# Kernel tuning notes

Measured on AMD Instinct MI355X. Metric: run time of the kernel, lower is better.

Reference implementation:

```python
import jax, jax.numpy as jnp
import numpy as np

B = 4096          # batch_size
D = 256           # embedding dim
N = 2 * B
TEMPERATURE = 0.5
GAMMA = 2.0
ALPHA = 0.25


def _negative_indices():
    # Static column indices of negatives per row: all columns except self (i)
    # and the positive partner ((i+B) mod N). Shape (N, N-2).
    idx = []
    for i in range(N):
        partner = (i + B) % N
        cols = [j for j in range(N) if j != i and j != partner]
        idx.append(cols)
    return np.asarray(idx, dtype=np.int32)

_NEG_IDX = jnp.asarray(_negative_indices())


def setup_inputs() -> dict:
    key = jax.random.key(0)
    kx, ky = jax.random.split(key)
    zx = jax.random.normal(kx, (B, D), dtype=jnp.float32)
    zy = jax.random.normal(ky, (B, D), dtype=jnp.float32)
    return {"zx": zx, "zy": zy}


def reference(zx, zy):
    z = jnp.concatenate([zx, zy], axis=0)                    # (N, D)
    zn = z / jnp.linalg.norm(z, axis=1, keepdims=True)       # cosine normalize
    sim = (zn @ zn.T) / TEMPERATURE                          # (N, N)

    sim_xy = jnp.diagonal(sim, offset=B)                     # (B,)
    sim_yx = jnp.diagonal(sim, offset=-B)                    # (B,)
    pos = jnp.concatenate([sim_xy, sim_yx])[:, None]         # (N, 1)
    neg = jnp.take_along_axis(sim, _NEG_IDX, axis=1)         # (N, N-2)

    logits = jnp.concatenate([pos, neg], axis=1)             # (N, N-1)
    # CE with label 0 for every row: -log_softmax(logits)[:, 0]
    ce = jax.nn.logsumexp(logits, axis=1) - logits[:, 0]
    pt = jnp.exp(-ce)
    focal = (1.0 - pt) ** GAMMA * ce
    return (ALPHA * focal).mean()
```

## Files before the change

### kernel.cpp

```cpp
#include <hip/hip_runtime.h>
#include <stdint.h>
#include <stddef.h>


typedef __attribute__((ext_vector_type(8))) short short8;
typedef __attribute__((ext_vector_type(4))) float f32x4;

#define NROWS 8192
#define DDIM 256
#define NTILES 2080

__device__ __forceinline__ unsigned short f2bf(float f) {
  unsigned int u = __float_as_uint(f);
  u = (u + 0x7FFFu + ((u >> 16) & 1u)) >> 16;
  return (unsigned short)u;
}

__global__ __launch_bounds__(256) void norm_kernel(const float* __restrict__ zx,
                                                   const float* __restrict__ zy,
                                                   unsigned short* __restrict__ zn) {
  const int row = blockIdx.x * 4 + (threadIdx.x >> 6);
  const int lane = threadIdx.x & 63;
  const float* src = (row < 4096) ? (zx + (size_t)row * DDIM)
                                  : (zy + (size_t)(row - 4096) * DDIM);
  float4 v = reinterpret_cast<const float4*>(src)[lane];
  float ss = v.x * v.x + v.y * v.y + v.z * v.z + v.w * v.w;
#pragma unroll
  for (int m = 1; m < 64; m <<= 1) ss += __shfl_xor(ss, m);
  const float sc = 1.41421356237f * rsqrtf(ss);
  ushort4 o;
  o.x = f2bf(v.x * sc); o.y = f2bf(v.y * sc);
  o.z = f2bf(v.z * sc); o.w = f2bf(v.w * sc);
  reinterpret_cast<ushort4*>(zn + (size_t)row * DDIM)[lane] = o;
}

__global__ __launch_bounds__(256, 2) void simtri_kernel(const unsigned short* __restrict__ zn,
                                                        float* __restrict__ partial,
                                                        float* __restrict__ pos) {
  __shared__ unsigned short smem[2][2][128 * 64];
  const int bid = blockIdx.x;
  int p = (int)((129.0f - sqrtf((float)(16641 - 8 * bid))) * 0.5f);
  p = max(0, min(63, p));
  while ((((p + 1) * (129 - (p + 1))) >> 1) <= bid) ++p;
  while (((p * (129 - p)) >> 1) > bid) --p;
  const int q = p + (bid - ((p * (129 - p)) >> 1));
  const int R0 = p << 7;
  const int C0 = q << 7;
  const bool isdiag = (p == q);
  const bool ispos = (q == p + 32);

  const int tid = threadIdx.x;
  const int lane = tid & 63;
  const int wid = tid >> 6;
  const int wr = wid >> 1;
  const int wc = wid & 1;

  const f32x4 z4 = {0.f, 0.f, 0.f, 0.f};
  f32x4 acc[4][4];
#pragma unroll
  for (int m = 0; m < 4; ++m)
#pragma unroll
    for (int n = 0; n < 4; ++n) acc[m][n] = z4;

  auto stage = [&](int buf, int which, int row0, int k0) {
    unsigned short* lb = &smem[buf][which][0];
#pragma unroll
    for (int j = 0; j < 4; ++j) {
      const int u = j * 256 + wid * 64 + lane;
      const unsigned short* g = zn + (size_t)(row0 + (u >> 3)) * DDIM + k0 + (u & 7) * 8;
      unsigned short* l = lb + (size_t)(j * 256 + wid * 64) * 8;
      __builtin_amdgcn_global_load_lds(
          (const __attribute__((address_space(1))) void*)g,
          (__attribute__((address_space(3))) void*)l, 16, 0, 0);
    }
  };

  stage(0, 0, R0, 0);
  if (!isdiag) stage(0, 1, C0, 0);
  __syncthreads();

  int buf = 0;
#pragma unroll
  for (int s = 0; s < 4; ++s) {
    if (s < 3) {
      stage(buf ^ 1, 0, R0, (s + 1) * 64);
      if (!isdiag) stage(buf ^ 1, 1, C0, (s + 1) * 64);
    }
    const unsigned short* A = &smem[buf][0][0];
    const unsigned short* Bm = isdiag ? A : &smem[buf][1][0];
#pragma unroll
    for (int ks = 0; ks < 2; ++ks) {
      short8 af[4], bfr[4];
#pragma unroll
      for (int m = 0; m < 4; ++m)
        af[m] = *reinterpret_cast<const short8*>(
            A + ((wr * 64 + m * 16 + (lane & 15)) * 64 + ks * 32 + (lane >> 4) * 8));
#pragma unroll
      for (int n = 0; n < 4; ++n)
        bfr[n] = *reinterpret_cast<const short8*>(
            Bm + ((wc * 64 + n * 16 + (lane & 15)) * 64 + ks * 32 + (lane >> 4) * 8));
#pragma unroll
      for (int m = 0; m < 4; ++m)
#pragma unroll
        for (int n = 0; n < 4; ++n)
          acc[m][n] = __builtin_amdgcn_mfma_f32_16x16x32_bf16(af[m], bfr[n], acc[m][n], 0, 0, 0);
    }
    buf ^= 1;
    __syncthreads();
  }

  float rsum[4][4];
  float csum[4];
#pragma unroll
  for (int m = 0; m < 4; ++m)
#pragma unroll
    for (int r = 0; r < 4; ++r) rsum[m][r] = 0.f;
#pragma unroll
  for (int n = 0; n < 4; ++n) csum[n] = 0.f;

#pragma unroll
  for (int m = 0; m < 4; ++m) {
    const int grow_b = R0 + wr * 64 + m * 16 + ((lane >> 4) << 2);
#pragma unroll
    for (int n = 0; n < 4; ++n) {
      const int gcol = C0 + wc * 64 + n * 16 + (lane & 15);
#pragma unroll
      for (int r = 0; r < 4; ++r) {
        const int grow = grow_b + r;
        const float val = acc[m][n][r];
        if (ispos && (gcol == grow + 4096)) pos[grow] = val;
        const float e = (isdiag && (grow == gcol)) ? 0.f : __expf(val);
        rsum[m][r] += e;
        csum[n] += e;
      }
    }
  }

#pragma unroll
  for (int m = 0; m < 4; ++m)
#pragma unroll
    for (int r = 0; r < 4; ++r) {
      float s = rsum[m][r];
      s += __shfl_xor(s, 1); s += __shfl_xor(s, 2);
      s += __shfl_xor(s, 4); s += __shfl_xor(s, 8);
      if ((lane & 15) == 0) {
        const int grow = R0 + wr * 64 + m * 16 + ((lane >> 4) << 2) + r;
        partial[(size_t)(q * 2 + wc) * NROWS + grow] = s;
      }
    }

  if (!isdiag) {
#pragma unroll
    for (int n = 0; n < 4; ++n) {
      float c = csum[n];
      c += __shfl_xor(c, 16); c += __shfl_xor(c, 32);
      if (lane < 16)
        partial[(size_t)(p * 2 + wr) * NROWS + (C0 + wc * 64 + n * 16 + lane)] = c;
    }
  }
}

__global__ __launch_bounds__(256) void d1_kernel(const float* __restrict__ partial,
                                                 const float* __restrict__ pos,
                                                 float* __restrict__ bsum) {
  const int row = blockIdx.x * 256 + threadIdx.x;
  float s = 0.f;
#pragma unroll 16
  for (int c = 0; c < 128; ++c) s += partial[(size_t)c * NROWS + row];
  const float ce = __logf(s) - pos[row & 4095];
  const float pt = __expf(-ce);
  float f = (1.f - pt) * (1.f - pt) * ce;
#pragma unroll
  for (int m = 1; m < 64; m <<= 1) f += __shfl_xor(f, m);
  __shared__ float wsum[4];
  if ((threadIdx.x & 63) == 0) wsum[threadIdx.x >> 6] = f;
  __syncthreads();
  if (threadIdx.x == 0) bsum[blockIdx.x] = wsum[0] + wsum[1] + wsum[2] + wsum[3];
}

__global__ __launch_bounds__(64) void d2_kernel(const float* __restrict__ bsum,
                                                float* __restrict__ out) {
  const int l = threadIdx.x;
  float v = (l < 32) ? bsum[l] : 0.f;
#pragma unroll
  for (int m = 1; m < 64; m <<= 1) v += __shfl_xor(v, m);
  if (l == 0) out[0] = 0.25f * v / 8192.f;
}

extern "C" void kernel_launch(void* const* d_in, const int* in_sizes, int n_in,
                              void* d_out, int out_size, void* d_ws, size_t ws_size,
                              hipStream_t stream) {
  const float* zx = (const float*)d_in[0];
  const float* zy = (const float*)d_in[1];
  float* out = (float*)d_out;

  unsigned short* zn = (unsigned short*)d_ws;
  float* pos = (float*)((char*)d_ws + (size_t)NROWS * DDIM * 2);
  float* partial = pos + 4096;
  float* bsum = partial + (size_t)128 * NROWS;

  norm_kernel<<<2048, 256, 0, stream>>>(zx, zy, zn);
  simtri_kernel<<<NTILES, 256, 0, stream>>>(zn, partial, pos);
  d1_kernel<<<32, 256, 0, stream>>>(partial, pos, bsum);
  d2_kernel<<<1, 64, 0, stream>>>(bsum, out);
}
```

Measured before the change: 112.6 us.

## Persistent tile loop with cross-tile prefetch, exp2 scaling, fused final reduction

The similarity kernel becomes persistent: 512 blocks each walk 4-5 triangular tiles and prefetch the next tile's first K-slice while the current tile finishes. Before this, 2080 short-lived blocks each paid their own prologue and epilogue. The normalization scale now folds in log2(e), so the kernel can use a raw exp2, and the diagonal and positive-pair handling moves out of the per-element loop into a targeted correction. The last reduction kernel is merged into d1 through an atomic counter that norm_kernel resets. This removes one launch but relies on the counter reset ordering and on a fixed tile distribution across 256 CUs.

```diff
diff --git a/kernel.cpp b/kernel.cpp
--- a/kernel.cpp
+++ b/kernel.cpp
@@ -9,6 +9,7 @@
 #define NROWS 8192
 #define DDIM 256
 #define NTILES 2080
+#define NBLK 512
 
 __device__ __forceinline__ unsigned short f2bf(float f) {
   unsigned int u = __float_as_uint(f);
@@ -16,9 +17,20 @@
   return (unsigned short)u;
 }
 
+__device__ __forceinline__ void unrank_tile(int t, int& p_out, int& q_out) {
+  int p = (int)((129.0f - sqrtf((float)(16641 - 8 * t))) * 0.5f);
+  p = max(0, min(63, p));
+  while ((((p + 1) * (129 - (p + 1))) >> 1) <= t) ++p;
+  while (((p * (129 - p)) >> 1) > t) --p;
+  p_out = p;
+  q_out = p + (t - ((p * (129 - p)) >> 1));
+}
+
 __global__ __launch_bounds__(256) void norm_kernel(const float* __restrict__ zx,
                                                    const float* __restrict__ zy,
-                                                   unsigned short* __restrict__ zn) {
+                                                   unsigned short* __restrict__ zn,
+                                                   unsigned int* __restrict__ counter) {
+  if (blockIdx.x == 0 && threadIdx.x == 0) *counter = 0u;
   const int row = blockIdx.x * 4 + (threadIdx.x >> 6);
   const int lane = threadIdx.x & 63;
   const float* src = (row < 4096) ? (zx + (size_t)row * DDIM)
@@ -27,7 +39,7 @@
   float ss = v.x * v.x + v.y * v.y + v.z * v.z + v.w * v.w;
 #pragma unroll
   for (int m = 1; m < 64; m <<= 1) ss += __shfl_xor(ss, m);
-  const float sc = 1.41421356237f * rsqrtf(ss);
+  const float sc = 1.69864360f * rsqrtf(ss);
   ushort4 o;
   o.x = f2bf(v.x * sc); o.y = f2bf(v.y * sc);
   o.z = f2bf(v.z * sc); o.w = f2bf(v.w * sc);
@@ -39,16 +51,7 @@
                                                         float* __restrict__ pos) {
   __shared__ unsigned short smem[2][2][128 * 64];
   const int bid = blockIdx.x;
-  int p = (int)((129.0f - sqrtf((float)(16641 - 8 * bid))) * 0.5f);
-  p = max(0, min(63, p));
-  while ((((p + 1) * (129 - (p + 1))) >> 1) <= bid) ++p;
-  while (((p * (129 - p)) >> 1) > bid) --p;
-  const int q = p + (bid - ((p * (129 - p)) >> 1));
-  const int R0 = p << 7;
-  const int C0 = q << 7;
-  const bool isdiag = (p == q);
-  const bool ispos = (q == p + 32);
-
+  const int nt = (bid < NTILES - NBLK * 4) ? 5 : 4;
   const int tid = threadIdx.x;
   const int lane = tid & 63;
   const int wid = tid >> 6;
@@ -62,7 +65,7 @@
 #pragma unroll
     for (int n = 0; n < 4; ++n) acc[m][n] = z4;
 
-  auto stage = [&](int buf, int which, int row0, int k0) {
+  auto stage_one = [&](int buf, int which, int row0, int k0) {
     unsigned short* lb = &smem[buf][which][0];
 #pragma unroll
     for (int j = 0; j < 4; ++j) {
@@ -74,117 +77,147 @@
           (__attribute__((address_space(3))) void*)l, 16, 0, 0);
     }
   };
-
-  stage(0, 0, R0, 0);
-  if (!isdiag) stage(0, 1, C0, 0);
+  auto stageT = [&](int buf, int p, int q, int k0) {
+    stage_one(buf, 0, p << 7, k0);
+    if (p != q) stage_one(buf, 1, q << 7, k0);
+  };
+
+  int cp, cq;
+  unrank_tile(bid, cp, cq);
+  stageT(0, cp, cq, 0);
   __syncthreads();
 
   int buf = 0;
-#pragma unroll
-  for (int s = 0; s < 4; ++s) {
-    if (s < 3) {
-      stage(buf ^ 1, 0, R0, (s + 1) * 64);
-      if (!isdiag) stage(buf ^ 1, 1, C0, (s + 1) * 64);
-    }
-    const unsigned short* A = &smem[buf][0][0];
-    const unsigned short* Bm = isdiag ? A : &smem[buf][1][0];
-#pragma unroll
-    for (int ks = 0; ks < 2; ++ks) {
-      short8 af[4], bfr[4];
+  for (int i = 0; i < nt; ++i) {
+    int np = cp, nq = cq;
+    const bool have_next = (i + 1 < nt);
+    if (have_next) unrank_tile(bid + NBLK * (i + 1), np, nq);
+    const bool isdiag = (cp == cq);
+    const bool ispos = (cq == cp + 32);
+    const int R0 = cp << 7;
+    const int C0 = cq << 7;
+
+#pragma unroll
+    for (int kk = 0; kk < 4; ++kk) {
+      if (kk < 3) stageT(buf ^ 1, cp, cq, (kk + 1) * 64);
+      else if (have_next) stageT(buf ^ 1, np, nq, 0);
+      const unsigned short* A = &smem[buf][0][0];
+      const unsigned short* Bm = isdiag ? A : &smem[buf][1][0];
+#pragma unroll
+      for (int ks = 0; ks < 2; ++ks) {
+        short8 af[4], bfr[4];
+#pragma unroll
+        for (int m = 0; m < 4; ++m)
+          af[m] = *reinterpret_cast<const short8*>(
+              A + ((wr * 64 + m * 16 + (lane & 15)) * 64 + ks * 32 + (lane >> 4) * 8));
+#pragma unroll
+        for (int n = 0; n < 4; ++n)
+          bfr[n] = *reinterpret_cast<const short8*>(
+              Bm + ((wc * 64 + n * 16 + (lane & 15)) * 64 + ks * 32 + (lane >> 4) * 8));
+#pragma unroll
+        for (int m = 0; m < 4; ++m)
+#pragma unroll
+          for (int n = 0; n < 4; ++n)
+            acc[m][n] = __builtin_amdgcn_mfma_f32_16x16x32_bf16(af[m], bfr[n], acc[m][n], 0, 0, 0);
+      }
+      buf ^= 1;
+      if (kk < 3) __syncthreads();
+    }
+
+    float rsum[4][4];
+    float csum[4];
+#pragma unroll
+    for (int m = 0; m < 4; ++m)
+#pragma unroll
+      for (int r = 0; r < 4; ++r) rsum[m][r] = 0.f;
+#pragma unroll
+    for (int n = 0; n < 4; ++n) csum[n] = 0.f;
+
+#pragma unroll
+    for (int m = 0; m < 4; ++m)
+#pragma unroll
+      for (int n = 0; n < 4; ++n)
+#pragma unroll
+        for (int r = 0; r < 4; ++r) {
+          const float e = __builtin_amdgcn_exp2f(acc[m][n][r]);
+          rsum[m][r] += e;
+          csum[n] += e;
+        }
+
+    if ((isdiag || ispos) && (wr == wc)) {
+      const int hi = lane >> 4, lo = lane & 15;
 #pragma unroll
       for (int m = 0; m < 4; ++m)
-        af[m] = *reinterpret_cast<const short8*>(
-            A + ((wr * 64 + m * 16 + (lane & 15)) * 64 + ks * 32 + (lane >> 4) * 8));
-#pragma unroll
-      for (int n = 0; n < 4; ++n)
-        bfr[n] = *reinterpret_cast<const short8*>(
-            Bm + ((wc * 64 + n * 16 + (lane & 15)) * 64 + ks * 32 + (lane >> 4) * 8));
-#pragma unroll
-      for (int m = 0; m < 4; ++m)
-#pragma unroll
-        for (int n = 0; n < 4; ++n)
-          acc[m][n] = __builtin_amdgcn_mfma_f32_16x16x32_bf16(af[m], bfr[n], acc[m][n], 0, 0, 0);
-    }
-    buf ^= 1;
+#pragma unroll
+        for (int r = 0; r < 4; ++r)
+          if (lo == 4 * hi + r) {
+            if (isdiag) rsum[m][r] -= __builtin_amdgcn_exp2f(acc[m][m][r]);
+            else        pos[R0 + wr * 64 + m * 16 + lo] = acc[m][m][r];
+          }
+    }
+
+#pragma unroll
+    for (int m = 0; m < 4; ++m)
+#pragma unroll
+      for (int r = 0; r < 4; ++r) {
+        float s = rsum[m][r];
+        s += __shfl_xor(s, 1); s += __shfl_xor(s, 2);
+        s += __shfl_xor(s, 4); s += __shfl_xor(s, 8);
+        if ((lane & 15) == 0) {
+          const int grow = R0 + wr * 64 + m * 16 + ((lane >> 4) << 2) + r;
+          partial[(size_t)(cq * 2 + wc) * NROWS + grow] = s;
+        }
+      }
+
+    if (!isdiag) {
+#pragma unroll
+      for (int n = 0; n < 4; ++n) {
+        float c = csum[n];
+        c += __shfl_xor(c, 16); c += __shfl_xor(c, 32);
+        if (lane < 16)
+          partial[(size_t)(cp * 2 + wr) * NROWS + (C0 + wc * 64 + n * 16 + lane)] = c;
+      }
+    }
+
+#pragma unroll
+    for (int m = 0; m < 4; ++m)
+#pragma unroll
+      for (int n = 0; n < 4; ++n) acc[m][n] = z4;
+
     __syncthreads();
-  }
-
-  float rsum[4][4];
-  float csum[4];
-#pragma unroll
-  for (int m = 0; m < 4; ++m)
-#pragma unroll
-    for (int r = 0; r < 4; ++r) rsum[m][r] = 0.f;
-#pragma unroll
-  for (int n = 0; n < 4; ++n) csum[n] = 0.f;
-
-#pragma unroll
-  for (int m = 0; m < 4; ++m) {
-    const int grow_b = R0 + wr * 64 + m * 16 + ((lane >> 4) << 2);
-#pragma unroll
-    for (int n = 0; n < 4; ++n) {
-      const int gcol = C0 + wc * 64 + n * 16 + (lane & 15);
-#pragma unroll
-      for (int r = 0; r < 4; ++r) {
-        const int grow = grow_b + r;
-        const float val = acc[m][n][r];
-        if (ispos && (gcol == grow + 4096)) pos[grow] = val;
-        const float e = (isdiag && (grow == gcol)) ? 0.f : __expf(val);
-        rsum[m][r] += e;
-        csum[n] += e;
-      }
-    }
-  }
-
-#pragma unroll
-  for (int m = 0; m < 4; ++m)
-#pragma unroll
-    for (int r = 0; r < 4; ++r) {
-      float s = rsum[m][r];
-      s += __shfl_xor(s, 1); s += __shfl_xor(s, 2);
-      s += __shfl_xor(s, 4); s += __shfl_xor(s, 8);
-      if ((lane & 15) == 0) {
-        const int grow = R0 + wr * 64 + m * 16 + ((lane >> 4) << 2) + r;
-        partial[(size_t)(q * 2 + wc) * NROWS + grow] = s;
-      }
-    }
-
-  if (!isdiag) {
-#pragma unroll
-    for (int n = 0; n < 4; ++n) {
-      float c = csum[n];
-      c += __shfl_xor(c, 16); c += __shfl_xor(c, 32);
-      if (lane < 16)
-        partial[(size_t)(p * 2 + wr) * NROWS + (C0 + wc * 64 + n * 16 + lane)] = c;
-    }
+    cp = np; cq = nq;
   }
 }
 
 __global__ __launch_bounds__(256) void d1_kernel(const float* __restrict__ partial,
                                                  const float* __restrict__ pos,
-                                                 float* __restrict__ bsum) {
+                                                 float* __restrict__ bsum,
+                                                 float* __restrict__ out,
+                                                 unsigned int* __restrict__ counter) {
   const int row = blockIdx.x * 256 + threadIdx.x;
   float s = 0.f;
 #pragma unroll 16
   for (int c = 0; c < 128; ++c) s += partial[(size_t)c * NROWS + row];
-  const float ce = __logf(s) - pos[row & 4095];
-  const float pt = __expf(-ce);
+  const float L = __log2f(s) - pos[row & 4095];
+  const float pt = __builtin_amdgcn_exp2f(-L);
+  const float ce = 0.69314718056f * L;
   float f = (1.f - pt) * (1.f - pt) * ce;
 #pragma unroll
   for (int m = 1; m < 64; m <<= 1) f += __shfl_xor(f, m);
   __shared__ float wsum[4];
   if ((threadIdx.x & 63) == 0) wsum[threadIdx.x >> 6] = f;
   __syncthreads();
-  if (threadIdx.x == 0) bsum[blockIdx.x] = wsum[0] + wsum[1] + wsum[2] + wsum[3];
-}
-
-__global__ __launch_bounds__(64) void d2_kernel(const float* __restrict__ bsum,
-                                                float* __restrict__ out) {
-  const int l = threadIdx.x;
-  float v = (l < 32) ? bsum[l] : 0.f;
-#pragma unroll
-  for (int m = 1; m < 64; m <<= 1) v += __shfl_xor(v, m);
-  if (l == 0) out[0] = 0.25f * v / 8192.f;
+  if (threadIdx.x == 0) {
+    bsum[blockIdx.x] = wsum[0] + wsum[1] + wsum[2] + wsum[3];
+    __threadfence();
+    if (atomicAdd(counter, 1u) == 31u) {
+      __threadfence();
+      float v = 0.f;
+#pragma unroll
+      for (int c = 0; c < 32; ++c) v += ((const volatile float*)bsum)[c];
+      out[0] = 0.25f * v / 8192.f;
+    }
+  }
 }
 
 extern "C" void kernel_launch(void* const* d_in, const int* in_sizes, int n_in,
@@ -198,9 +231,9 @@
   float* pos = (float*)((char*)d_ws + (size_t)NROWS * DDIM * 2);
   float* partial = pos + 4096;
   float* bsum = partial + (size_t)128 * NROWS;
-
-  norm_kernel<<<2048, 256, 0, stream>>>(zx, zy, zn);
-  simtri_kernel<<<NTILES, 256, 0, stream>>>(zn, partial, pos);
-  d1_kernel<<<32, 256, 0, stream>>>(partial, pos, bsum);
-  d2_kernel<<<1, 64, 0, stream>>>(bsum, out);
-}
+  unsigned int* counter = (unsigned int*)(bsum + 32);
+
+  norm_kernel<<<2048, 256, 0, stream>>>(zx, zy, zn, counter);
+  simtri_kernel<<<NBLK, 256, 0, stream>>>(zn, partial, pos);
+  d1_kernel<<<32, 256, 0, stream>>>(partial, pos, bsum, out, counter);
+}
```

New measurement: 110.2 us. 2.1% less time.
